# Optimization experiments

Measured on AMD Instinct MI355X. Metric: run time of the kernel, lower is better.

## Reference

```python
import jax, jax.numpy as jnp
import numpy as np
import math

B, NRES, RPR = 1, 384, 3
L = NRES * RPR          # 1152 rigids
CS, CZ = 256, 128
CH, H, PQ, PV = 16, 8, 8, 12


def _ln(x, scale, bias):
    mu = jnp.mean(x, axis=-1, keepdims=True)
    var = jnp.var(x, axis=-1, keepdims=True)
    return (x - mu) * jax.lax.rsqrt(var + 1e-5) * scale + bias


def _quat_to_rot(q):
    q = q / jnp.linalg.norm(q, axis=-1, keepdims=True)
    w, x, y, z = q[..., 0], q[..., 1], q[..., 2], q[..., 3]
    r = jnp.stack([
        1 - 2 * (y * y + z * z), 2 * (x * y - w * z), 2 * (x * z + w * y),
        2 * (x * y + w * z), 1 - 2 * (x * x + z * z), 2 * (y * z - w * x),
        2 * (x * z - w * y), 2 * (y * z + w * x), 1 - 2 * (x * x + y * y),
    ], axis=-1)
    return r.reshape(q.shape[:-1] + (3, 3))


def setup_inputs() -> dict:
    key = jax.random.key(0)
    ks = jax.random.split(key, 20)
    s = jax.random.normal(ks[0], (B, L, CS), jnp.float32)
    z = jax.random.normal(ks[1], (B, NRES, NRES, CZ), jnp.float32)
    rot = _quat_to_rot(jax.random.normal(ks[2], (B, L, 4), jnp.float32))
    trans = 10.0 * jax.random.normal(ks[3], (B, L, 3), jnp.float32)
    mask = jnp.ones((B, L), jnp.float32)
    rigid_to_res_idx = jnp.broadcast_to(jnp.arange(L, dtype=jnp.int32) // RPR, (B, L))
    w = lambda k, sh: 0.02 * jax.random.normal(k, sh, jnp.float32)
    return {
        "s": s, "z": z, "rot": rot, "trans": trans, "mask": mask,
        "ln_s_scale": jnp.ones((CS,), jnp.float32), "ln_s_bias": jnp.zeros((CS,), jnp.float32),
        "ln_z_scale": jnp.ones((CZ,), jnp.float32), "ln_z_bias": jnp.zeros((CZ,), jnp.float32),
        "w_q": w(ks[4], (CS, H * CH)), "w_k": w(ks[5], (CS, H * CH)), "w_v": w(ks[6], (CS, H * CH)),
        "w_qp": w(ks[7], (CS, H * PQ * 3)), "w_kp": w(ks[8], (CS, H * PQ * 3)), "w_vp": w(ks[9], (CS, H * PV * 3)),
        "w_b": w(ks[10], (CZ, H)),
        "head_weights": jnp.full((H,), 0.5413, jnp.float32),  # softplus^-1(1)
        "w_out": w(ks[11], (H * (CH + CZ + PV * 4), CS)),
        "b_out": jnp.zeros((CS,), jnp.float32),
        "rigid_to_res_idx": rigid_to_res_idx,
    }


def reference(s, z, rot, trans, mask, ln_s_scale, ln_s_bias, ln_z_scale, ln_z_bias,
              w_q, w_k, w_v, w_qp, w_kp, w_vp, w_b, head_weights, w_out, b_out,
              rigid_to_res_idx):
    b_, l_ = s.shape[0], s.shape[1]
    idx = rigid_to_res_idx[0]                       # [L] rigid -> residue, shared over batch
    s_ln = _ln(s, ln_s_scale, ln_s_bias)            # [B,L,CS]
    z_ln = _ln(z, ln_z_scale, ln_z_bias)            # [B,N,N,CZ]

    q = (s_ln @ w_q).reshape(b_, l_, H, CH)
    k = (s_ln @ w_k).reshape(b_, l_, H, CH)
    v = (s_ln @ w_v).reshape(b_, l_, H, CH)

    # local points, then rigid-transform to global frame: x_g = R x + t
    q_p = (s_ln @ w_qp).reshape(b_, l_, H, PQ, 3)
    k_p = (s_ln @ w_kp).reshape(b_, l_, H, PQ, 3)
    v_p = (s_ln @ w_vp).reshape(b_, l_, H, PV, 3)
    t5 = trans[:, :, None, None, :]
    q_g = jnp.einsum("blij,blhpj->blhpi", rot, q_p) + t5
    k_g = jnp.einsum("blij,blhpj->blhpi", rot, k_p) + t5
    v_g = jnp.einsum("blij,blhpj->blhpi", rot, v_p) + t5

    # scalar qk term
    a = jnp.einsum("blhc,bjhc->bhlj", q, k) * math.sqrt(1.0 / (3 * CH))
    # pair bias, broadcast residue-pair -> rigid-pair
    b_res = z_ln @ w_b                                # [B,N,N,H]
    b_full = b_res[:, idx][:, :, idx]                 # [B,L,L,H]
    a = a + math.sqrt(1.0 / 3) * jnp.transpose(b_full, (0, 3, 1, 2))
    # point-distance term: ||q-k||^2 = |q|^2 + |k|^2 - 2 q.k (summed over P,3)
    hw = jax.nn.softplus(head_weights) * math.sqrt(1.0 / (3 * (PQ * 9.0 / 2)))
    qq = jnp.sum(q_g * q_g, axis=(-1, -2)).transpose(0, 2, 1)   # [B,H,L]
    kk = jnp.sum(k_g * k_g, axis=(-1, -2)).transpose(0, 2, 1)
    qk = jnp.einsum("blhpc,bjhpc->bhlj", q_g, k_g)
    d2 = qq[:, :, :, None] + kk[:, :, None, :] - 2.0 * qk
    a = a - 0.5 * d2 * hw[None, :, None, None]
    a = a + (mask[:, None, None, :] - 1.0) * 1e9
    attn = jax.nn.softmax(a, axis=-1)                 # [B,H,L,L]

    o = jnp.einsum("bhlj,bjhc->blhc", attn, v)        # [B,L,H,CH]
    o_pt_g = jnp.einsum("bhlj,bjhpc->blhpc", attn, v_g)
    # back to local frame of query rigid: R^T (x - t)
    o_pt = jnp.einsum("blji,blhpj->blhpi", rot, o_pt_g - t5)
    o_pt_norm = jnp.sqrt(jnp.sum(o_pt * o_pt, axis=-1) + 1e-8)  # [B,L,H,PV]
    # pair output: sum attention over rigids belonging to each key residue
    attn_res = attn.reshape(b_, H, l_, NRES, RPR).sum(-1)       # [B,H,L,N]
    z_l = z_ln[:, idx]                                           # [B,L,N,CZ]
    o_pair = jnp.einsum("bhln,blnc->blhc", attn_res, z_l)        # [B,L,H,CZ]

    cat = jnp.concatenate(
        [o, o_pt.reshape(b_, l_, H, PV * 3), o_pt_norm, o_pair], axis=-1
    ).reshape(b_, l_, H * (CH + PV * 4 + CZ))
    return cat @ w_out + b_out                        # [B,L,CS]
```

## Files before the change

kernel.cpp:

```cpp
#include <hip/hip_runtime.h>
#include <hip/hip_bf16.h>

#define L 1152
#define NRES 384
#define CS 256
#define CZ 128
#define H 8
#define CH 16
#define PQ 8
#define PV 12
#define PSTR 1088

#define OFF_SLN  0L
#define OFF_PROJ 294912L
#define OFF_WPK  1548288L
#define OFF_QCAT 1826816L
#define OFF_KCAT 2232320L
#define OFF_VCAT 2637824L
#define OFF_BRES 3227648L
#define OFF_MURS 4407296L
#define OFF_ATTN 4702208L
#define OFF_CAT  15319040L
#define OFF_PCAT 17088512L
#define OFF_RSTAT 18268160L
#define OFF_PAV  18286592L
#define OFF_POP  21825536L

__global__ __launch_bounds__(256) void k_ln_s(const float* s, const float* sc, const float* bi, float* sln){
  int l = blockIdx.x, t = threadIdx.x;
  __shared__ float red[CS];
  float x = s[(long)l*CS + t];
  red[t] = x; __syncthreads();
  for(int st=128; st>0; st>>=1){ if(t<st) red[t]+=red[t+st]; __syncthreads(); }
  float mu = red[0] * (1.f/CS); __syncthreads();
  float d = x - mu;
  red[t] = d*d; __syncthreads();
  for(int st=128; st>0; st>>=1){ if(t<st) red[t]+=red[t+st]; __syncthreads(); }
  float var = red[0]*(1.f/CS);
  sln[(long)l*CS + t] = d*rsqrtf(var + 1e-5f)*sc[t] + bi[t];
}

__global__ __launch_bounds__(256) void k_packw(const float* wq, const float* wk, const float* wv,
                        const float* wqp, const float* wkp, const float* wvp, float* wpack){
  int k = blockIdx.x, t = threadIdx.x;
  for(int c=t; c<PSTR; c+=256){
    float v;
    if(c<128)        v = wq [(long)k*128 + c];
    else if(c<256)   v = wk [(long)k*128 + c-128];
    else if(c<384)   v = wv [(long)k*128 + c-256];
    else if(c<576)   v = wqp[(long)k*192 + c-384];
    else if(c<768)   v = wkp[(long)k*192 + c-576];
    else if(c<1056)  v = wvp[(long)k*288 + c-768];
    else             v = 0.f;
    wpack[(long)k*PSTR + c] = v;
  }
}

__global__ __launch_bounds__(256) void k_proj(const float* sln, const float* wpack, float* proj){
  int l0 = blockIdx.x*64, c0 = blockIdx.y*64, t = threadIdx.x;
  __shared__ float a_s[32][68];
  __shared__ __align__(16) float w_s[32][68];
  int tr = t>>4, tc = t&15;
  float4 acc[4] = {{0,0,0,0},{0,0,0,0},{0,0,0,0},{0,0,0,0}};
  for(int kc=0; kc<8; kc++){
    int k0 = kc*32;
    {
      int row = t>>2, kk0 = (t&3)*8;
      const float4* src = (const float4*)(sln + (long)(l0+row)*256 + k0 + kk0);
      float4 v0 = src[0], v1 = src[1];
      a_s[kk0+0][row]=v0.x; a_s[kk0+1][row]=v0.y; a_s[kk0+2][row]=v0.z; a_s[kk0+3][row]=v0.w;
      a_s[kk0+4][row]=v1.x; a_s[kk0+5][row]=v1.y; a_s[kk0+6][row]=v1.z; a_s[kk0+7][row]=v1.w;
    }
    #pragma unroll
    for(int kk2=0; kk2<2; kk2++){
      int kk = (t>>4) + 16*kk2;
      *(float4*)&w_s[kk][(t&15)*4] = *(const float4*)(wpack + (long)(k0+kk)*PSTR + c0 + (t&15)*4);
    }
    __syncthreads();
    #pragma unroll 8
    for(int kk=0; kk<32; kk++){
      float4 a4 = *(const float4*)&a_s[kk][tr*4];
      float4 b4 = *(const float4*)&w_s[kk][tc*4];
      acc[0].x+=a4.x*b4.x; acc[0].y+=a4.x*b4.y; acc[0].z+=a4.x*b4.z; acc[0].w+=a4.x*b4.w;
      acc[1].x+=a4.y*b4.x; acc[1].y+=a4.y*b4.y; acc[1].z+=a4.y*b4.z; acc[1].w+=a4.y*b4.w;
      acc[2].x+=a4.z*b4.x; acc[2].y+=a4.z*b4.y; acc[2].z+=a4.z*b4.z; acc[2].w+=a4.z*b4.w;
      acc[3].x+=a4.w*b4.x; acc[3].y+=a4.w*b4.y; acc[3].z+=a4.w*b4.z; acc[3].w+=a4.w*b4.w;
    }
    __syncthreads();
  }
  #pragma unroll
  for(int r=0;r<4;r++)
    *(float4*)(proj + (long)(l0 + tr*4 + r)*PSTR + c0 + tc*4) = acc[r];
}

__global__ __launch_bounds__(256) void k_ln_z(const float* z, const float* sc, const float* bi,
                       const float* wb, float* murs, float* bres_t){
  int t = threadIdx.x;
  long rp0 = (long)blockIdx.x*32;
  int r = t>>3, part = t&7;
  long rp = rp0 + r;
  __shared__ __align__(16) float swb[8*132];
  __shared__ float SB[8][2];
  const float4* z4 = (const float4*)z;
  float4 x0 = z4[rp*32 + part*4 + 0];
  float4 x1 = z4[rp*32 + part*4 + 1];
  float4 x2 = z4[rp*32 + part*4 + 2];
  float4 x3 = z4[rp*32 + part*4 + 3];
  #pragma unroll
  for(int k2=0;k2<4;k2++){
    int e = t + k2*256; int h = e>>7, c = e&127;
    swb[h*132 + c] = sc[c]*wb[(long)c*8 + h];
  }
  __syncthreads();
  if(t < 64){
    int h = t>>3, seg = t&7;
    float S=0, Bv=0;
    #pragma unroll
    for(int i=0;i<16;i++){
      int c = seg*16+i;
      S  += swb[h*132+c];
      Bv += bi[c]*wb[(long)c*8 + h];
    }
    #pragma unroll
    for(int off=1;off<8;off<<=1){ S += __shfl_xor(S,off,64); Bv += __shfl_xor(Bv,off,64); }
    if(seg==0){ SB[h][0]=S; SB[h][1]=Bv; }
  }
  float s1 = x0.x+x0.y+x0.z+x0.w + x1.x+x1.y+x1.z+x1.w
           + x2.x+x2.y+x2.z+x2.w + x3.x+x3.y+x3.z+x3.w;
  float s2 = x0.x*x0.x+x0.y*x0.y+x0.z*x0.z+x0.w*x0.w
           + x1.x*x1.x+x1.y*x1.y+x1.z*x1.z+x1.w*x1.w
           + x2.x*x2.x+x2.y*x2.y+x2.z*x2.z+x2.w*x2.w
           + x3.x*x3.x+x3.y*x3.y+x3.z*x3.z+x3.w*x3.w;
  #pragma unroll
  for(int off=1;off<8;off<<=1){ s1 += __shfl_xor(s1,off,64); s2 += __shfl_xor(s2,off,64); }
  float mu = s1*(1.f/CZ);
  float var = s2*(1.f/CZ) - mu*mu;
  float rstd = rsqrtf(var + 1e-5f);
  if(part==0){ murs[rp*2]=mu; murs[rp*2+1]=rstd; }
  float acc[8];
  const float4* swb4 = (const float4*)swb;
  #pragma unroll
  for(int h=0;h<8;h++){
    float4 wa = swb4[h*33 + part*4 + 0];
    float4 wbv= swb4[h*33 + part*4 + 1];
    float4 wc = swb4[h*33 + part*4 + 2];
    float4 wd = swb4[h*33 + part*4 + 3];
    acc[h] = x0.x*wa.x + x0.y*wa.y + x0.z*wa.z + x0.w*wa.w
           + x1.x*wbv.x+ x1.y*wbv.y+ x1.z*wbv.z+ x1.w*wbv.w
           + x2.x*wc.x + x2.y*wc.y + x2.z*wc.z + x2.w*wc.w
           + x3.x*wd.x + x3.y*wd.y + x3.z*wd.z + x3.w*wd.w;
  }
  #pragma unroll
  for(int off=1;off<8;off<<=1){
    #pragma unroll
    for(int h=0;h<8;h++) acc[h] += __shfl_xor(acc[h],off,64);
  }
  __syncthreads();
  if(part==0){
    #pragma unroll
    for(int h=0;h<8;h++)
      bres_t[(long)h*147456 + rp] = rstd*(acc[h] - mu*SB[h][0]) + SB[h][1];
  }
}

__global__ __launch_bounds__(256) void k_rigid(const float* proj, const float* rot, const float* trans,
                        const float* mask, const float* hws,
                        float* qcat, float* kcat, float* vcat){
  int l = blockIdx.x, t = threadIdx.x;
  __shared__ float R[9], T[3], hwS[8], qgs[192], kgs[192];
  if(t<9) R[t]=rot[(long)l*9+t];
  if(t<3) T[t]=trans[(long)l*3+t];
  if(t>=16 && t<24) hwS[t-16] = log1pf(expf(hws[t-16]))*0.09622504486493764f;
  __syncthreads();
  const float* pr = proj + (long)l*PSTR;
  if(t<128){
    int h=t>>4, c=t&15;
    long base = ((long)h*L + l)*44;
    qcat[base + c] = 0.14433756729740643f * pr[t];
    kcat[base + c] = pr[128+t];
    vcat[((long)h*L + l)*64 + c] = pr[256+t];
  }
  if(t < 192){
    int h=t/24, m=t%24, p=m/3, i=m%3;
    float qa = R[i*3+0]*pr[384+h*24+p*3+0] + R[i*3+1]*pr[384+h*24+p*3+1]
             + R[i*3+2]*pr[384+h*24+p*3+2] + T[i];
    float ka = R[i*3+0]*pr[576+h*24+p*3+0] + R[i*3+1]*pr[576+h*24+p*3+1]
             + R[i*3+2]*pr[576+h*24+p*3+2] + T[i];
    qgs[t]=qa; kgs[t]=ka;
    long base = ((long)h*L + l)*44 + 16 + m;
    qcat[base] = hwS[h]*qa;
    kcat[base] = ka;
  }
  for(int it=t; it<288; it+=256){
    int h=it/36, m=it%36, p=m/3, i=m%3;
    float a = R[i*3+0]*pr[768+h*36+p*3+0] + R[i*3+1]*pr[768+h*36+p*3+1]
            + R[i*3+2]*pr[768+h*36+p*3+2] + T[i];
    vcat[((long)h*L + l)*64 + 16 + m] = a;
  }
  if(t < 96){
    int h=t/12, d=t%12;
    vcat[((long)h*L + l)*64 + 52 + d] = 0.f;
  }
  __syncthreads();
  if(t < 8){
    float qq=0, kk=0;
    #pragma unroll
    for(int m=0;m<24;m++){ qq += qgs[t*24+m]*qgs[t*24+m]; kk += kgs[t*24+m]*kgs[t*24+m]; }
    long base = ((long)t*L + l)*44;
    qcat[base + 40] = -0.5f*hwS[t]*qq;
    kcat[base + 40] = -0.5f*hwS[t]*kk + (mask[l]-1.f)*1e9f;
  }
}

__global__ __launch_bounds__(256) void k_scores(const float* qcat, const float* kcat,
                         const float* bres_t, const int* ridx, float* attn){
  int l0 = blockIdx.x*32, j0 = blockIdx.y*64, h = blockIdx.z;
  int t = threadIdx.x;
  __shared__ __align__(16) float q_s[32*44];
  __shared__ __align__(16) float k_s[64*44];
  __shared__ int rj_s[64];
  {
    const float* srcq = qcat + ((long)h*L + l0)*44;
    for(int i=t; i<32*44; i+=256) q_s[i]=srcq[i];
    const float* srck = kcat + ((long)h*L + j0)*44;
    for(int i=t; i<64*44; i+=256) k_s[i]=srck[i];
    if(t<64) rj_s[t]=ridx[j0+t];
  }
  __syncthreads();
  int a = t>>5;
  int b = t&31;
  float acc[4][2] = {{0,0},{0,0},{0,0},{0,0}};
  const float4* q4 = (const float4*)q_s;
  const float4* k4 = (const float4*)k_s;
  #pragma unroll
  for(int i=0;i<10;i++){
    float4 kA = k4[(long)b*11 + i];
    float4 kB = k4[(long)(b+32)*11 + i];
    #pragma unroll
    for(int r=0;r<4;r++){
      float4 qv = q4[(long)(a+8*r)*11 + i];
      acc[r][0] += qv.x*kA.x + qv.y*kA.y + qv.z*kA.z + qv.w*kA.w;
      acc[r][1] += qv.x*kB.x + qv.y*kB.y + qv.z*kB.z + qv.w*kB.w;
    }
  }
  float colc0 = k_s[b*44+40], colc1 = k_s[(b+32)*44+40];
  int rj0 = rj_s[b], rj1 = rj_s[b+32];
  const float* bbh = bres_t + (long)h*147456;
  #pragma unroll
  for(int r=0;r<4;r++){
    int row = a+8*r;
    float rowc = q_s[row*44+40];
    int rl = ridx[l0+row];
    const float* bb = bbh + (long)rl*NRES;
    float s0 = acc[r][0] + rowc + colc0 + 0.5773502691896258f*bb[rj0];
    float s1 = acc[r][1] + rowc + colc1 + 0.5773502691896258f*bb[rj1];
    float* arow = attn + ((long)h*L + l0+row)*L + j0;
    arow[b]    = s0;
    arow[b+32] = s1;
  }
}

__global__ __launch_bounds__(256) void k_rowstat(const float* attn, float* rowstat){
  long row = (long)blockIdx.x*4 + (threadIdx.x>>6);
  int lane = threadIdx.x & 63;
  const float* p = attn + row*L;
  float v[18];
  float m=-1e30f;
  #pragma unroll
  for(int i=0;i<18;i++){ v[i]=p[lane + i*64]; m=fmaxf(m,v[i]); }
  #pragma unroll
  for(int off=1;off<64;off<<=1) m=fmaxf(m,__shfl_xor(m,off,64));
  float s=0;
  #pragma unroll
  for(int i=0;i<18;i++) s+=__expf(v[i]-m);
  #pragma unroll
  for(int off=1;off<64;off<<=1) s+=__shfl_xor(s,off,64);
  if(lane==0){ rowstat[row*2]=m; rowstat[row*2+1]=1.f/s; }
}

__global__ __launch_bounds__(256) void k_av(const float* attn, const float* vcat,
                     const float* rowstat, float* pav){
  int lb = blockIdx.x, h = blockIdx.y, sp = blockIdx.z, t = threadIdx.x;
  int l0 = lb*32;
  __shared__ float a_s[64][33];
  __shared__ __align__(16) float v_s[64][68];
  int lgrp = t>>4, dgrp = t&15;
  float4 acc0 = {0,0,0,0}, acc1 = {0,0,0,0};
  const float* abase = attn + ((long)h*L + l0)*L;
  int al = t>>3, jj0 = (t&7)*8;
  float mrow = rowstat[((long)h*L + l0 + al)*2];
  float irow = rowstat[((long)h*L + l0 + al)*2 + 1];
  for(int jc=sp*3; jc<sp*3+3; jc++){
    int j0 = jc*64;
    {
      const float4* src = (const float4*)(abase + (long)al*L + j0 + jj0);
      float4 p0 = src[0], p1 = src[1];
      a_s[jj0+0][al]=__expf(p0.x-mrow)*irow;
      a_s[jj0+1][al]=__expf(p0.y-mrow)*irow;
      a_s[jj0+2][al]=__expf(p0.z-mrow)*irow;
      a_s[jj0+3][al]=__expf(p0.w-mrow)*irow;
      a_s[jj0+4][al]=__expf(p1.x-mrow)*irow;
      a_s[jj0+5][al]=__expf(p1.y-mrow)*irow;
      a_s[jj0+6][al]=__expf(p1.z-mrow)*irow;
      a_s[jj0+7][al]=__expf(p1.w-mrow)*irow;
    }
    {
      int jj = t>>2, seg = t&3;
      const float4* src = (const float4*)(vcat + ((long)h*L + j0 + jj)*64 + seg*16);
      float4 q0=src[0], q1=src[1], q2=src[2], q3=src[3];
      float4* dst = (float4*)&v_s[jj][seg*16];
      dst[0]=q0; dst[1]=q1; dst[2]=q2; dst[3]=q3;
    }
    __syncthreads();
    #pragma unroll 8
    for(int jj=0; jj<64; jj++){
      float a0 = a_s[jj][lgrp*2], a1 = a_s[jj][lgrp*2+1];
      const float4 vv = *(const float4*)&v_s[jj][dgrp*4];
      acc0.x+=a0*vv.x; acc0.y+=a0*vv.y; acc0.z+=a0*vv.z; acc0.w+=a0*vv.w;
      acc1.x+=a1*vv.x; acc1.y+=a1*vv.y; acc1.z+=a1*vv.z; acc1.w+=a1*vv.w;
    }
    __syncthreads();
  }
  float* dst = pav + (((long)sp*H + h)*L + l0 + lgrp*2)*64 + dgrp*4;
  *(float4*)dst = acc0;
  *(float4*)(dst + 64) = acc1;
}

__global__ __launch_bounds__(256) void k_avred(const float* pav, const float* rot, const float* trans,
                        float* cat){
  int lb = blockIdx.x, h = blockIdx.y, t = threadIdx.x;
  int l0 = lb*32;
  __shared__ __align__(16) float fin_s[32][64];
  #pragma unroll
  for(int k=0;k<2;k++){
    int fi = t + k*256;
    int l = fi>>4, c4 = fi&15;
    long base = (((long)h)*L + l0 + l)*64 + c4*4;
    float4 r = {0,0,0,0};
    #pragma unroll
    for(int p=0;p<6;p++){
      float4 a = *(const float4*)(pav + (long)p*589824 + base);
      r.x+=a.x; r.y+=a.y; r.z+=a.z; r.w+=a.w;
    }
    *(float4*)&fin_s[l][c4*4] = r;
  }
  __syncthreads();
  for(int it=t; it<32*16; it+=256){
    int l=it>>4, c=it&15;
    cat[(long)(l0+l)*1536 + h*192 + c] = fin_s[l][c];
  }
  for(int it=t; it<32*12; it+=256){
    int l=it/12, p=it%12;
    long gl = l0+l;
    float og0 = fin_s[l][16+p*3+0]-trans[gl*3+0];
    float og1 = fin_s[l][16+p*3+1]-trans[gl*3+1];
    float og2 = fin_s[l][16+p*3+2]-trans[gl*3+2];
    float* crow = cat + gl*1536 + h*192;
    float nrm=0;
    #pragma unroll
    for(int i=0;i<3;i++){
      float v = rot[gl*9+0+i]*og0 + rot[gl*9+3+i]*og1 + rot[gl*9+6+i]*og2;
      crow[16+p*3+i]=v; nrm+=v*v;
    }
    crow[52+p]=sqrtf(nrm+1e-8f);
  }
}

__global__ __launch_bounds__(256) void k_opair(const float* attn, const float* z, const float* murs,
                        const float* rowstat,
                        const float* sc, const float* bi, const int* ridx, float* po){
  int r=blockIdx.x, sp=blockIdx.y, t=threadIdx.x;
  __shared__ __align__(16) float ar[3][H][96];
  __shared__ __align__(16) float mrs[96*2];
  __shared__ float rs_s[24][2];
  int rl = ridx[r*3];
  int n0 = sp*96;
  if(t<24){
    int lo=t/8, h=t%8;
    long row = (long)h*L + r*3+lo;
    rs_s[t][0]=rowstat[row*2]; rs_s[t][1]=rowstat[row*2+1];
  }
  __syncthreads();
  for(int it=t; it<3*H*96; it+=256){
    int lo = it/(H*96);
    int rem = it - lo*(H*96);
    int h = rem/96, n = rem - h*96;
    const float* arow = attn + ((long)h*L + r*3+lo)*L + (n0+n)*3;
    float m = rs_s[lo*8+h][0], iv = rs_s[lo*8+h][1];
    ar[lo][h][n]=(__expf(arow[0]-m)+__expf(arow[1]-m)+__expf(arow[2]-m))*iv;
  }
  for(int i=t;i<96*2;i+=256) mrs[i]=murs[((long)rl*NRES + n0)*2 + i];
  __syncthreads();
  int tc=t&63, th=t>>6;
  int c0=tc*2, h0=th*2;
  float sc0=sc[c0], sc1=sc[c0+1], bi0=bi[c0], bi1=bi[c0+1];
  float acc[3][2][2]={};
  const float* zbase = z + ((long)(rl*NRES + n0))*CZ + c0;
  for(int n=0;n<96;n+=2){
    float4 mr4 = *(const float4*)&mrs[n*2];
    float2 z0 = *(const float2*)(zbase + (long)n*CZ);
    float2 z1 = *(const float2*)(zbase + (long)(n+1)*CZ);
    float zv00 = (z0.x - mr4.x)*mr4.y*sc0 + bi0;
    float zv01 = (z0.y - mr4.x)*mr4.y*sc1 + bi1;
    float zv10 = (z1.x - mr4.z)*mr4.w*sc0 + bi0;
    float zv11 = (z1.y - mr4.z)*mr4.w*sc1 + bi1;
    #pragma unroll
    for(int lo=0;lo<3;lo++){
      #pragma unroll
      for(int hp=0;hp<2;hp++){
        float2 a2 = *(const float2*)&ar[lo][h0+hp][n];
        acc[lo][hp][0] += a2.x*zv00 + a2.y*zv10;
        acc[lo][hp][1] += a2.x*zv01 + a2.y*zv11;
      }
    }
  }
  #pragma unroll
  for(int lo=0;lo<3;lo++){
    float* prow = po + ((long)sp*L + r*3+lo)*1024;
    #pragma unroll
    for(int hp=0;hp<2;hp++){
      float2 w = {acc[lo][hp][0], acc[lo][hp][1]};
      *(float2*)&prow[(h0+hp)*128 + c0] = w;
    }
  }
}

__global__ __launch_bounds__(256) void k_opred(const float* po, float* cat){
  int i = blockIdx.x*256 + threadIdx.x;
  const float4* p = (const float4*)po;
  float4 a = p[i], b = p[i + 294912], c = p[i + 589824], d = p[i + 884736];
  int l = i>>8, rem = i&255;
  int h = rem>>5, c4 = rem&31;
  float4 r = {a.x+b.x+c.x+d.x, a.y+b.y+c.y+d.y, a.z+b.z+c.z+d.z, a.w+b.w+c.w+d.w};
  ((float4*)cat)[(long)l*384 + h*48 + 16 + c4] = r;
}

__global__ __launch_bounds__(256) void k_final(const float* cat, const float* wout, float* pcat){
  int l0 = blockIdx.x*32, c0 = blockIdx.y*32, kp = blockIdx.z, t = threadIdx.x;
  __shared__ float a_s[64][33];
  __shared__ __align__(16) float w_s[64][36];
  int tr = t>>3, tc = t&7;
  float4 acc = {0,0,0,0};
  for(int kc=0; kc<6; kc++){
    int k0 = kp*384 + kc*64;
    {
      int row = t>>3, kk0 = (t&7)*8;
      const float4* src = (const float4*)(cat + (long)(l0+row)*1536 + k0 + kk0);
      float4 v0 = src[0], v1 = src[1];
      a_s[kk0+0][row]=v0.x; a_s[kk0+1][row]=v0.y; a_s[kk0+2][row]=v0.z; a_s[kk0+3][row]=v0.w;
      a_s[kk0+4][row]=v1.x; a_s[kk0+5][row]=v1.y; a_s[kk0+6][row]=v1.z; a_s[kk0+7][row]=v1.w;
    }
    #pragma unroll
    for(int kk2=0; kk2<2; kk2++){
      int kk = (t>>3) + 32*kk2;
      *(float4*)&w_s[kk][(t&7)*4] = *(const float4*)(wout + (long)(k0+kk)*256 + c0 + (t&7)*4);
    }
    __syncthreads();
    #pragma unroll 8
    for(int kk=0; kk<64; kk++){
      float a0 = a_s[kk][tr];
      float4 b4 = *(const float4*)&w_s[kk][tc*4];
      acc.x+=a0*b4.x; acc.y+=a0*b4.y; acc.z+=a0*b4.z; acc.w+=a0*b4.w;
    }
    __syncthreads();
  }
  *(float4*)(pcat + ((long)kp*L + l0+tr)*256 + c0 + tc*4) = acc;
}

__global__ __launch_bounds__(256) void k_redout(const float* pcat, const float* bout, float* out){
  int i = blockIdx.x*256 + threadIdx.x;
  const float4* p = (const float4*)pcat;
  float4 a = p[i], b = p[i+73728], c = p[i+147456], d = p[i+221184];
  float4 bv = ((const float4*)bout)[i&63];
  float4 r;
  r.x = a.x+b.x+c.x+d.x+bv.x;
  r.y = a.y+b.y+c.y+d.y+bv.y;
  r.z = a.z+b.z+c.z+d.z+bv.z;
  r.w = a.w+b.w+c.w+d.w+bv.w;
  ((float4*)out)[i] = r;
}

extern "C" void kernel_launch(void* const* d_in, const int* in_sizes, int n_in,
                              void* d_out, int out_size, void* d_ws, size_t ws_size,
                              hipStream_t stream) {
  const float* s      = (const float*)d_in[0];
  const float* z      = (const float*)d_in[1];
  const float* rot    = (const float*)d_in[2];
  const float* trans  = (const float*)d_in[3];
  const float* mask   = (const float*)d_in[4];
  const float* lnss   = (const float*)d_in[5];
  const float* lnsb   = (const float*)d_in[6];
  const float* lnzs   = (const float*)d_in[7];
  const float* lnzb   = (const float*)d_in[8];
  const float* wq     = (const float*)d_in[9];
  const float* wk     = (const float*)d_in[10];
  const float* wv     = (const float*)d_in[11];
  const float* wqp    = (const float*)d_in[12];
  const float* wkp    = (const float*)d_in[13];
  const float* wvp    = (const float*)d_in[14];
  const float* wb     = (const float*)d_in[15];
  const float* hws    = (const float*)d_in[16];
  const float* wout   = (const float*)d_in[17];
  const float* bout   = (const float*)d_in[18];
  const int*  ridx    = (const int*)d_in[19];

  float* ws  = (float*)d_ws;
  float* out = (float*)d_out;

  float* sln  = ws + OFF_SLN;
  float* proj = ws + OFF_PROJ;
  float* wpk  = ws + OFF_WPK;
  float* qcat = ws + OFF_QCAT;
  float* kcat = ws + OFF_KCAT;
  float* vcat = ws + OFF_VCAT;
  float* bres = ws + OFF_BRES;
  float* murs = ws + OFF_MURS;
  float* attn = ws + OFF_ATTN;
  float* cat  = ws + OFF_CAT;
  float* pcat = ws + OFF_PCAT;
  float* rstat= ws + OFF_RSTAT;
  float* pav  = ws + OFF_PAV;
  float* po   = ws + OFF_POP;

  k_packw<<<dim3(256), dim3(256), 0, stream>>>(wq, wk, wv, wqp, wkp, wvp, wpk);
  k_ln_s<<<dim3(L), dim3(CS), 0, stream>>>(s, lnss, lnsb, sln);
  k_proj<<<dim3(18,17), dim3(256), 0, stream>>>(sln, wpk, proj);
  k_ln_z<<<dim3(NRES*NRES/32), dim3(256), 0, stream>>>(z, lnzs, lnzb, wb, murs, bres);
  k_rigid<<<dim3(L), dim3(256), 0, stream>>>(proj, rot, trans, mask, hws, qcat, kcat, vcat);
  k_scores<<<dim3(L/32, L/64, H), dim3(256), 0, stream>>>(qcat, kcat, bres, ridx, attn);
  k_rowstat<<<dim3(H*L/4), dim3(256), 0, stream>>>(attn, rstat);
  k_av<<<dim3(L/32, H, 6), dim3(256), 0, stream>>>(attn, vcat, rstat, pav);
  k_avred<<<dim3(L/32, H), dim3(256), 0, stream>>>(pav, rot, trans, cat);
  k_opair<<<dim3(NRES, 4), dim3(256), 0, stream>>>(attn, z, murs, rstat, lnzs, lnzb, ridx, po);
  k_opred<<<dim3(1152), dim3(256), 0, stream>>>(po, cat);
  k_final<<<dim3(36,8,4), dim3(256), 0, stream>>>(cat, wout, pcat);
  k_redout<<<dim3(288), dim3(256), 0, stream>>>(pcat, bout, out);
}
```

Measured before the change: 333.2 us.

## Fold z layer-norm algebraically out of opair inner loop and register-prefetch z rows

The pair-output kernel no longer normalises z inside its inner loop. The per-key inverse std is folded into the attention weights, the mean term is subtracted through a precomputed per-row dot product, the scale is applied once at the end, and the bias is added in the reduction kernel, which works because the pooled attention rows sum to one across all splits. The inner loop is rewritten with float4 z loads covering 4 channels and one head per thread, using software double-buffered prefetch of z rows. This adds a small shuffle reduction and relies on the softmax rows summing to one across the four splits for the bias to be correct.

```diff
diff --git a/kernel.cpp b/kernel.cpp
--- a/kernel.cpp
+++ b/kernel.cpp
@@ -366,20 +366,45 @@
   }
 }
 
+#define OPAIR_STEP(Z0,Z1,Z2,Z3,NB) { \
+    float4 a0 = *(const float4*)&ar[0][th][NB]; \
+    float4 a1 = *(const float4*)&ar[1][th][NB]; \
+    float4 a2 = *(const float4*)&ar[2][th][NB]; \
+    acc[0][0] += a0.x*Z0.x + a0.y*Z1.x + a0.z*Z2.x + a0.w*Z3.x; \
+    acc[0][1] += a0.x*Z0.y + a0.y*Z1.y + a0.z*Z2.y + a0.w*Z3.y; \
+    acc[0][2] += a0.x*Z0.z + a0.y*Z1.z + a0.z*Z2.z + a0.w*Z3.z; \
+    acc[0][3] += a0.x*Z0.w + a0.y*Z1.w + a0.z*Z2.w + a0.w*Z3.w; \
+    acc[1][0] += a1.x*Z0.x + a1.y*Z1.x + a1.z*Z2.x + a1.w*Z3.x; \
+    acc[1][1] += a1.x*Z0.y + a1.y*Z1.y + a1.z*Z2.y + a1.w*Z3.y; \
+    acc[1][2] += a1.x*Z0.z + a1.y*Z1.z + a1.z*Z2.z + a1.w*Z3.z; \
+    acc[1][3] += a1.x*Z0.w + a1.y*Z1.w + a1.z*Z2.w + a1.w*Z3.w; \
+    acc[2][0] += a2.x*Z0.x + a2.y*Z1.x + a2.z*Z2.x + a2.w*Z3.x; \
+    acc[2][1] += a2.x*Z0.y + a2.y*Z1.y + a2.z*Z2.y + a2.w*Z3.y; \
+    acc[2][2] += a2.x*Z0.z + a2.y*Z1.z + a2.z*Z2.z + a2.w*Z3.z; \
+    acc[2][3] += a2.x*Z0.w + a2.y*Z1.w + a2.z*Z2.w + a2.w*Z3.w; }
+
 __global__ __launch_bounds__(256) void k_opair(const float* attn, const float* z, const float* murs,
                         const float* rowstat,
-                        const float* sc, const float* bi, const int* ridx, float* po){
+                        const float* sc, const int* ridx, float* po){
   int r=blockIdx.x, sp=blockIdx.y, t=threadIdx.x;
   __shared__ __align__(16) float ar[3][H][96];
   __shared__ __align__(16) float mrs[96*2];
   __shared__ float rs_s[24][2];
+  __shared__ float S1s[24];
   int rl = ridx[r*3];
   int n0 = sp*96;
+  int tc = t&31, th = t>>5;
+  const float* zbase = z + ((long)(rl*NRES + n0))*CZ + tc*4;
+  float4 zc0 = *(const float4*)(zbase + 0L*CZ);
+  float4 zc1 = *(const float4*)(zbase + 1L*CZ);
+  float4 zc2 = *(const float4*)(zbase + 2L*CZ);
+  float4 zc3 = *(const float4*)(zbase + 3L*CZ);
   if(t<24){
     int lo=t/8, h=t%8;
     long row = (long)h*L + r*3+lo;
     rs_s[t][0]=rowstat[row*2]; rs_s[t][1]=rowstat[row*2+1];
   }
+  for(int i=t;i<192;i+=256) mrs[i]=murs[((long)rl*NRES + n0)*2 + i];
   __syncthreads();
   for(int it=t; it<3*H*96; it+=256){
     int lo = it/(H*96);
@@ -387,51 +412,60 @@
     int h = rem/96, n = rem - h*96;
     const float* arow = attn + ((long)h*L + r*3+lo)*L + (n0+n)*3;
     float m = rs_s[lo*8+h][0], iv = rs_s[lo*8+h][1];
-    ar[lo][h][n]=(__expf(arow[0]-m)+__expf(arow[1]-m)+__expf(arow[2]-m))*iv;
-  }
-  for(int i=t;i<96*2;i+=256) mrs[i]=murs[((long)rl*NRES + n0)*2 + i];
-  __syncthreads();
-  int tc=t&63, th=t>>6;
-  int c0=tc*2, h0=th*2;
-  float sc0=sc[c0], sc1=sc[c0+1], bi0=bi[c0], bi1=bi[c0+1];
-  float acc[3][2][2]={};
-  const float* zbase = z + ((long)(rl*NRES + n0))*CZ + c0;
-  for(int n=0;n<96;n+=2){
-    float4 mr4 = *(const float4*)&mrs[n*2];
-    float2 z0 = *(const float2*)(zbase + (long)n*CZ);
-    float2 z1 = *(const float2*)(zbase + (long)(n+1)*CZ);
-    float zv00 = (z0.x - mr4.x)*mr4.y*sc0 + bi0;
-    float zv01 = (z0.y - mr4.x)*mr4.y*sc1 + bi1;
-    float zv10 = (z1.x - mr4.z)*mr4.w*sc0 + bi0;
-    float zv11 = (z1.y - mr4.z)*mr4.w*sc1 + bi1;
-    #pragma unroll
-    for(int lo=0;lo<3;lo++){
-      #pragma unroll
-      for(int hp=0;hp<2;hp++){
-        float2 a2 = *(const float2*)&ar[lo][h0+hp][n];
-        acc[lo][hp][0] += a2.x*zv00 + a2.y*zv10;
-        acc[lo][hp][1] += a2.x*zv01 + a2.y*zv11;
-      }
-    }
-  }
+    ar[lo][h][n]=(__expf(arow[0]-m)+__expf(arow[1]-m)+__expf(arow[2]-m))*iv*mrs[n*2+1];
+  }
+  __syncthreads();
+  if(t<192){
+    int row=t>>3, seg=t&7;
+    const float* arr = ((const float*)ar) + row*96 + seg*12;
+    const float* mur = mrs + seg*24;
+    float s1=0;
+    #pragma unroll
+    for(int q2=0;q2<12;q2++) s1 += arr[q2]*mur[q2*2];
+    s1 += __shfl_xor(s1,1,64); s1 += __shfl_xor(s1,2,64); s1 += __shfl_xor(s1,4,64);
+    if(seg==0) S1s[row]=s1;
+  }
+  __syncthreads();
+  float acc[3][4]={};
+  for(int nb=0; nb<88; nb+=8){
+    float4 zn0 = *(const float4*)(zbase + (long)(nb+4)*CZ);
+    float4 zn1 = *(const float4*)(zbase + (long)(nb+5)*CZ);
+    float4 zn2 = *(const float4*)(zbase + (long)(nb+6)*CZ);
+    float4 zn3 = *(const float4*)(zbase + (long)(nb+7)*CZ);
+    OPAIR_STEP(zc0,zc1,zc2,zc3, nb);
+    zc0 = *(const float4*)(zbase + (long)(nb+ 8)*CZ);
+    zc1 = *(const float4*)(zbase + (long)(nb+ 9)*CZ);
+    zc2 = *(const float4*)(zbase + (long)(nb+10)*CZ);
+    zc3 = *(const float4*)(zbase + (long)(nb+11)*CZ);
+    OPAIR_STEP(zn0,zn1,zn2,zn3, nb+4);
+  }
+  {
+    float4 zn0 = *(const float4*)(zbase + 92L*CZ);
+    float4 zn1 = *(const float4*)(zbase + 93L*CZ);
+    float4 zn2 = *(const float4*)(zbase + 94L*CZ);
+    float4 zn3 = *(const float4*)(zbase + 95L*CZ);
+    OPAIR_STEP(zc0,zc1,zc2,zc3, 88);
+    OPAIR_STEP(zn0,zn1,zn2,zn3, 92);
+  }
+  float4 sc4 = *(const float4*)(sc + tc*4);
   #pragma unroll
   for(int lo=0;lo<3;lo++){
-    float* prow = po + ((long)sp*L + r*3+lo)*1024;
-    #pragma unroll
-    for(int hp=0;hp<2;hp++){
-      float2 w = {acc[lo][hp][0], acc[lo][hp][1]};
-      *(float2*)&prow[(h0+hp)*128 + c0] = w;
-    }
-  }
-}
-
-__global__ __launch_bounds__(256) void k_opred(const float* po, float* cat){
+    float s1v = S1s[lo*8+th];
+    float4 o = { sc4.x*(acc[lo][0]-s1v), sc4.y*(acc[lo][1]-s1v),
+                 sc4.z*(acc[lo][2]-s1v), sc4.w*(acc[lo][3]-s1v) };
+    *(float4*)(po + ((long)sp*L + (long)(r*3+lo))*1024 + th*128 + tc*4) = o;
+  }
+}
+
+__global__ __launch_bounds__(256) void k_opred(const float* po, const float* bi, float* cat){
   int i = blockIdx.x*256 + threadIdx.x;
   const float4* p = (const float4*)po;
   float4 a = p[i], b = p[i + 294912], c = p[i + 589824], d = p[i + 884736];
   int l = i>>8, rem = i&255;
   int h = rem>>5, c4 = rem&31;
-  float4 r = {a.x+b.x+c.x+d.x, a.y+b.y+c.y+d.y, a.z+b.z+c.z+d.z, a.w+b.w+c.w+d.w};
+  float4 bv = ((const float4*)bi)[c4];
+  float4 r = {a.x+b.x+c.x+d.x+bv.x, a.y+b.y+c.y+d.y+bv.y,
+              a.z+b.z+c.z+d.z+bv.z, a.w+b.w+c.w+d.w+bv.w};
   ((float4*)cat)[(long)l*384 + h*48 + 16 + c4] = r;
 }
 
@@ -531,8 +565,8 @@
   k_rowstat<<<dim3(H*L/4), dim3(256), 0, stream>>>(attn, rstat);
   k_av<<<dim3(L/32, H, 6), dim3(256), 0, stream>>>(attn, vcat, rstat, pav);
   k_avred<<<dim3(L/32, H), dim3(256), 0, stream>>>(pav, rot, trans, cat);
-  k_opair<<<dim3(NRES, 4), dim3(256), 0, stream>>>(attn, z, murs, rstat, lnzs, lnzb, ridx, po);
-  k_opred<<<dim3(1152), dim3(256), 0, stream>>>(po, cat);
+  k_opair<<<dim3(NRES, 4), dim3(256), 0, stream>>>(attn, z, murs, rstat, lnzs, ridx, po);
+  k_opred<<<dim3(1152), dim3(256), 0, stream>>>(po, lnzb, cat);
   k_final<<<dim3(36,8,4), dim3(256), 0, stream>>>(cat, wout, pcat);
   k_redout<<<dim3(288), dim3(256), 0, stream>>>(pcat, bout, out);
 }
```

After: 323.9 us. -2.8%, faster.
